# Optimization experiments

Measured on AMD Instinct MI355X. Metric: run time of the kernel, lower is better.

The kernel has to match this reference:

```python
import jax, jax.numpy as jnp
import numpy as np

THRESHOLD = 1.0
DECAY = 0.95
T, B, N_IN = 16, 512, 3072
S1, S2, S3 = 256, 256, 128
E = 8


def _lif_step(v, h):
    # LIF membrane update: decay, integrate, threshold-spike, soft reset.
    v = v * DECAY + h
    spk = (v >= THRESHOLD).astype(v.dtype)
    return spk, v - spk * THRESHOLD


def setup_inputs() -> dict:
    key = jax.random.key(0)
    k_seq, k1, k2, k3 = jax.random.split(key, 4)
    # Binary spike train input (rate-coded), shape (T, B, N_in)
    spike_seq = (jax.random.uniform(k_seq, (T, B, N_IN)) < 0.5).astype(jnp.float32)
    # Expert weights: nn.Linear weight layout is (out, in); init N(0, 0.05)
    W1 = 0.05 * jax.random.normal(k1, (E, S1, N_IN), dtype=jnp.float32)
    W2 = 0.05 * jax.random.normal(k2, (E, S2, S1), dtype=jnp.float32)
    W3 = 0.05 * jax.random.normal(k3, (E, S3, S2), dtype=jnp.float32)
    # Uniform gates 1/num_experts (requires_grad=False buffers in the original)
    g = jnp.full((E,), 1.0 / E, dtype=jnp.float32)
    return {"spike_seq": spike_seq, "W1": W1, "W2": W2, "W3": W3,
            "g1": g, "g2": g, "g3": g}


def reference(spike_seq, W1, W2, W3, g1, g2, g3):
    t, b = spike_seq.shape[0], spike_seq.shape[1]
    x = spike_seq.reshape(t, b, -1)
    e = W1.shape[0]
    dt = x.dtype
    v1 = jnp.zeros((e, b, W1.shape[1]), dt)
    v2 = jnp.zeros((e, b, W2.shape[1]), dt)
    v3 = jnp.zeros((e, b, W3.shape[1]), dt)

    def step(carry, xt):
        v1, v2, v3 = carry
        # stage 1: batched per-expert GEMM + LIF + gated combine
        h1 = jnp.einsum('bi,eoi->ebo', xt, W1)
        spk1, v1 = _lif_step(v1, h1)
        c1 = jnp.einsum('e,ebo->bo', g1, spk1)
        # stage 2
        h2 = jnp.einsum('bi,eoi->ebo', c1, W2)
        spk2, v2 = _lif_step(v2, h2)
        c2 = jnp.einsum('e,ebo->bo', g2, spk2)
        # stage 3
        h3 = jnp.einsum('bi,eoi->ebo', c2, W3)
        spk3, v3 = _lif_step(v3, h3)
        c3 = jnp.einsum('e,ebo->bo', g3, spk3)
        return (v1, v2, v3), (c1, c2, c3)

    _, (s1, s2, s3) = jax.lax.scan(step, (v1, v2, v3), x)
    # time-averaged combined outputs per stage
    return s1.mean(axis=0), s2.mean(axis=0), s3.mean(axis=0)
```

## Files before the change

kernel.cpp:

```cpp
#include <hip/hip_runtime.h>
#include <hip/hip_bf16.h>
#include <cmath>

#define T_STEPS 16
#define BATCH   512
#define N_IN    3072
#define S1      256
#define S2      256
#define S3      128
#define NEXP    8
#define M_ROWS  (T_STEPS * BATCH)
#define MT_ALL  (M_ROWS / 32)

typedef int v4i  __attribute__((ext_vector_type(4)));
typedef int v16i __attribute__((ext_vector_type(16)));
typedef unsigned long long u64;
typedef unsigned int uint32;

__device__ __forceinline__ v4i unpack16_bits(uint32 w16)
{
    v4i d;
    #pragma unroll
    for (int c = 0; c < 4; ++c) {
        uint32 x = (w16 >> (4 * c)) & 0xFu;
        x = x + (x << 7);
        x = x + (x << 14);
        d[c] = (int)(x & 0x01010101u);
    }
    return d;
}

template<int S, int K>
__device__ __forceinline__ void digitize_chunk(
    const float* __restrict__ W, char* __restrict__ Bf, int t)
{
    int lane16 = t & 63;
    int o  = (t >> 6) & (S - 1);
    int kb = t >> ((S == 256) ? 14 : 13);
    int r  = lane16 & 31;
    int qd = lane16 >> 5;
    int e    = r >> 2;
    int limb = r & 3;
    int k0 = kb * 32 + qd * 16;

    const float4* Wp = (const float4*)(W + ((size_t)e * S + o) * K + k0);
    char out[16];
    #pragma unroll
    for (int f4 = 0; f4 < 4; ++f4) {
        float4 w = Wp[f4];
        float ws[4] = {w.x, w.y, w.z, w.w};
        #pragma unroll
        for (int c = 0; c < 4; ++c) {
            long long q = llrint((double)ws[c] * 4294967296.0);
            int d = 0;
            #pragma unroll
            for (int l = 0; l < 4; ++l) {
                int dl = (int)((q + 128) & 255) - 128;
                q = (q - dl) >> 8;
                if (l == limb) d = dl;
            }
            out[f4 * 4 + c] = (char)d;
        }
    }
    *(v4i*)(Bf + (size_t)t * 16) = *(v4i*)out;
}

__global__ __launch_bounds__(256) void prep(
    const float* __restrict__ x,  const float* __restrict__ W1,
    const float* __restrict__ W2, const float* __restrict__ W3,
    u64* __restrict__ bitsT, char* __restrict__ B1f,
    char* __restrict__ B2f,  char* __restrict__ B3f)
{
    const int bid = blockIdx.x;
    const int tid = threadIdx.x;
    if (bid < 98304) {
        int gid = bid * 256 + tid;
        float v = x[gid];
        u64 m = __ballot(v >= 0.5f);
        if ((tid & 63) == 0) {
            int tb = gid / N_IN;
            int k  = gid - tb * N_IN;
            int t  = tb >> 9;
            int b  = tb & 511;
            bitsT[(size_t)(k >> 6) * M_ROWS + (b * 16 + t)] = m;
        }
    } else if (bid < 98304 + 4608) {
        int t    = (bid - 98304) * 256 + tid;
        int l16  = t & 63;
        int tt   = t >> 6;
        int tile = tt % 192;
        int kb   = tt / 192;
        int gr   = tile * 32 + (l16 & 31);
        int qd   = l16 >> 5;
        int limb = gr >> 11;
        int oe   = gr & 2047;
        int o    = oe >> 3;
        int e    = oe & 7;
        int k0   = kb * 32 + qd * 16;
        const float4* Wp = (const float4*)(W1 + ((size_t)e * S1 + o) * N_IN + k0);
        char out[16];
        #pragma unroll
        for (int f4 = 0; f4 < 4; ++f4) {
            float4 w = Wp[f4];
            float ws[4] = {w.x, w.y, w.z, w.w};
            #pragma unroll
            for (int c = 0; c < 4; ++c) {
                long long q = llrint((double)ws[c] * 16777216.0);
                int d0 = (int)((q + 128) & 255) - 128;
                long long q1 = (q - d0) >> 8;
                int d1 = (int)((q1 + 128) & 255) - 128;
                int d2 = (int)((q1 - d1) >> 8);
                int d  = (limb == 0) ? d0 : ((limb == 1) ? d1 : d2);
                out[f4 * 4 + c] = (char)d;
            }
        }
        *(v4i*)(B1f + (size_t)t * 16) = *(v4i*)out;
    } else if (bid < 98304 + 4608 + 512) {
        digitize_chunk<S2, S1>(W2, B2f, (bid - 98304 - 4608) * 256 + tid);
    } else {
        digitize_chunk<S3, S2>(W3, B3f, (bid - 98304 - 4608 - 512) * 256 + tid);
    }
}

__global__ __launch_bounds__(256, 3) void fused_stage1(
    const u64* __restrict__ AT0, const char* __restrict__ Bf,
    const float* __restrict__ g, char* __restrict__ Cf,
    float* __restrict__ Mean)
{
    constexpr int NGR = (N_IN / 32) / 4;
    __shared__ char smem[32768];
    double* hs  = (double*)smem;
    char*  Blds = smem;

    const int tid  = threadIdx.x;
    const int lane = tid & 63;
    const int w    = tid >> 6;
    const int col  = lane & 31;
    const int qd   = lane >> 5;
    const int sh16 = qd * 16;

    const int id    = blockIdx.x;
    const int xcd   = id & 7;
    const int inner = id >> 3;
    const int nblk  = xcd * 8 + (inner >> 5);
    const int mblk  = inner & 31;
    const int m0    = mblk * 256;

    const u64* AT = AT0 + (m0 + w * 64 + col);

    const char* Bsrc = Bf + (size_t)nblk * 1024 + lane * 16;
    char* Bdst0 = Blds + (w * 3) * 1024 + lane * 16;

    v16i acc[2][3];
    #pragma unroll
    for (int mt = 0; mt < 2; ++mt)
        #pragma unroll
        for (int jj = 0; jj < 3; ++jj)
            #pragma unroll
            for (int r = 0; r < 16; ++r) acc[mt][jj][r] = 0;

    u64 areg[2][4];

    auto stageB = [&](int gr, int buf) {
        const char* src = Bsrc + (size_t)(gr * 4 + w) * (192 * 1024);
        char* dst = Bdst0 + buf * 12288;
        #pragma unroll
        for (int jj = 0; jj < 3; ++jj)
            __builtin_amdgcn_global_load_lds(
                (const __attribute__((address_space(1))) uint32*)(src + jj * 65536),
                (__attribute__((address_space(3))) uint32*)(dst + jj * 1024),
                16, 0, 0);
    };
    auto loadA = [&](int gr, int buf) {
        const int kw = gr * 2;
        areg[buf][0] = AT[(size_t)kw * M_ROWS];
        areg[buf][1] = AT[(size_t)kw * M_ROWS + 32];
        areg[buf][2] = AT[(size_t)(kw + 1) * M_ROWS];
        areg[buf][3] = AT[(size_t)(kw + 1) * M_ROWS + 32];
    };

    stageB(0, 0);
    loadA(0, 0);

    auto iter = [&](int gr, int cur, int pf) {
        stageB(gr + 1, pf);
        loadA(gr + 1, pf);
        asm volatile("s_waitcnt vmcnt(7)" ::: "memory");
        __builtin_amdgcn_sched_barrier(0);
        __builtin_amdgcn_s_barrier();
        const char* bb = Blds + cur * 12288 + lane * 16;
        __builtin_amdgcn_s_setprio(1);
        #pragma unroll
        for (int kbl = 0; kbl < 4; ++kbl) {
            v4i Bfr[3];
            #pragma unroll
            for (int jj = 0; jj < 3; ++jj)
                Bfr[jj] = *(const v4i*)(bb + (kbl * 3 + jj) * 1024);
            const int kwl = kbl >> 1;
            v4i af[2];
            #pragma unroll
            for (int mt = 0; mt < 2; ++mt) {
                u64 a = areg[cur][kwl * 2 + mt];
                uint32 dw = (kbl & 1) ? (uint32)(a >> 32) : (uint32)a;
                af[mt] = unpack16_bits(dw >> sh16);
            }
            #pragma unroll
            for (int mt = 0; mt < 2; ++mt)
                #pragma unroll
                for (int jj = 0; jj < 3; ++jj)
                    acc[mt][jj] = __builtin_amdgcn_mfma_i32_32x32x32_i8(
                        af[mt], Bfr[jj], acc[mt][jj], 0, 0, 0);
        }
        __builtin_amdgcn_s_setprio(0);
        __builtin_amdgcn_s_barrier();
    };

    for (int gp = 0; gp < NGR; gp += 2) {
        iter(gp + 0, 0, 1);
        iter(gp + 1, 1, 0);
    }

    const double sc = 1.0 / 16777216.0;
    auto write_hs = [&](int wl) {
        #pragma unroll
        for (int mt = 0; mt < 2; ++mt)
            #pragma unroll
            for (int reg = 0; reg < 16; ++reg) {
                int r  = wl * 64 + mt * 32 + (reg & 3) + 8 * (reg >> 2) + 4 * qd;
                int lo = acc[mt][0][reg] + (acc[mt][1][reg] << 8);
                double d = ((double)lo + 65536.0 * (double)acc[mt][2][reg]) * sc;
                hs[r * 32 + col] = d;
            }
    };
    const int b_loc = tid >> 5;
    const int oe    = tid & 31;
    const int o_loc = oe >> 3;
    const int e     = tid & 7;
    const float ge  = g[e];
    const int og    = nblk * 4 + o_loc;
    const int kb_a   = og >> 5;
    const int qd_a   = (og >> 4) & 1;
    const int byte_a = og & 15;

    auto lif_pass = [&](int pass) {
        const int bg = mblk * 16 + pass * 8 + b_loc;
        double v = 0.0;
        float gacc = 0.0f;
        #pragma unroll
        for (int t = 0; t < T_STEPS; ++t) {
            double h  = hs[(b_loc * 16 + t) * 32 + oe];
            double vv = v * 0.95 + h;
            int spk = (vv >= 1.0) ? 1 : 0;
            v = vv - (double)spk;
            float gs = ge * (float)spk;
            gs += __shfl_xor(gs, 1);
            gs += __shfl_xor(gs, 2);
            gs += __shfl_xor(gs, 4);
            gacc += gs;
            int cnt = spk;
            cnt += __shfl_xor(cnt, 1);
            cnt += __shfl_xor(cnt, 2);
            cnt += __shfl_xor(cnt, 4);
            if (e == 0) {
                int mp = bg * 16 + t;
                int lane_a = (mp & 31) + 32 * qd_a;
                Cf[(((size_t)kb_a * MT_ALL + (mp >> 5)) * 64 + lane_a) * 16 + byte_a]
                    = (char)cnt;
            }
        }
        if (e == 0) Mean[(size_t)bg * S1 + og] = gacc * 0.0625f;
    };

    __syncthreads();
    if (w < 2) write_hs(w);
    __syncthreads();
    lif_pass(0);
    __syncthreads();
    if (w >= 2) write_hs(w - 2);
    __syncthreads();
    lif_pass(1);
}

template<int K, int S, int SHIFT, bool WRITEC, int NBLK, int MINW>
__global__ __launch_bounds__(256, MINW) void fused_stage(
    const char* __restrict__ Ap, const char* __restrict__ Bf,
    const float* __restrict__ g, char* __restrict__ Cf,
    float* __restrict__ Mean)
{
    constexpr int KI = K / 64;
    static_assert(KI % 2 == 0, "frag path wants even KI");
    constexpr int NT = S;
    constexpr int NS = NBLK / 8;
    __shared__ double hs[256][16];

    const int tid  = threadIdx.x;
    const int lane = tid & 63;
    const int w    = tid >> 6;
    const int col  = lane & 31;
    const int qd   = lane >> 5;
    const int wm   = w * 64;

    const int id    = blockIdx.x;
    const int xcd   = id & 7;
    const int inner = id >> 3;
    const int nblk  = xcd * NS + (inner >> 5);
    const int mblk  = inner & 31;
    const int m0    = mblk * 256;

    const int nt0 = nblk * 2;
    const char* Bbase = Bf + ((size_t)nt0 * 64 + lane) * 16;

    v16i acc[2][2];
    #pragma unroll
    for (int i = 0; i < 2; ++i)
        #pragma unroll
        for (int j = 0; j < 2; ++j)
            #pragma unroll
            for (int r = 0; r < 16; ++r) acc[i][j][r] = 0;

    auto loadB = [&](int kb, int jj) -> v4i {
        return *(const v4i*)(Bbase + (size_t)kb * (NT * 1024) + jj * 1024);
    };
    const int mt0 = (m0 + wm) >> 5;
    const char* Abase = Ap + ((size_t)mt0 * 64 + lane) * 16;
    auto loadA = [&](int kb, int ii) -> v4i {
        return *(const v4i*)(Abase + (size_t)kb * (MT_ALL * 1024) + ii * 1024);
    };

    v4i Ab[2][4];
    v4i Bb[2][4];

    #pragma unroll
    for (int ks = 0; ks < 2; ++ks) {
        Ab[0][ks * 2 + 0] = loadA(ks, 0);
        Ab[0][ks * 2 + 1] = loadA(ks, 1);
        #pragma unroll
        for (int jj = 0; jj < 2; ++jj)
            Bb[0][ks * 2 + jj] = loadB(ks, jj);
    }

    auto body = [&](int it, int cur, int pf) {
        const int itp = it + 1;
        #pragma unroll
        for (int ks = 0; ks < 2; ++ks) {
            Ab[pf][ks * 2 + 0] = loadA(itp * 2 + ks, 0);
            Ab[pf][ks * 2 + 1] = loadA(itp * 2 + ks, 1);
            #pragma unroll
            for (int jj = 0; jj < 2; ++jj)
                Bb[pf][ks * 2 + jj] = loadB(itp * 2 + ks, jj);
        }
        #pragma unroll
        for (int ks = 0; ks < 2; ++ks)
            #pragma unroll
            for (int jj = 0; jj < 2; ++jj) {
                acc[0][jj] = __builtin_amdgcn_mfma_i32_32x32x32_i8(Ab[cur][ks*2+0], Bb[cur][ks*2+jj], acc[0][jj], 0,0,0);
                acc[1][jj] = __builtin_amdgcn_mfma_i32_32x32x32_i8(Ab[cur][ks*2+1], Bb[cur][ks*2+jj], acc[1][jj], 0,0,0);
            }
    };
    for (int it = 0; it < KI; it += 2) {
        body(it + 0, 0, 1);
        body(it + 1, 1, 0);
    }

    const double sbase = 1.0 / (double)(1ll << SHIFT);
    #pragma unroll
    for (int j = 0; j < 2; ++j) {
        const int oe = j * 8 + (col >> 2);
        #pragma unroll
        for (int i = 0; i < 2; ++i) {
            #pragma unroll
            for (int reg = 0; reg < 16; ++reg) {
                int a = acc[i][j][reg];
                int s01 = a + (__shfl_xor(a, 1) << 8);
                int s23 = __shfl_xor(s01, 2);
                double d = ((double)s01 + 65536.0 * (double)s23) * sbase;
                if ((col & 3) == 0) {
                    int m = wm + i * 32 + (reg & 3) + 8 * (reg >> 2) + 4 * qd;
                    hs[m][oe] = d;
                }
            }
        }
    }
    __syncthreads();

    const int b_loc  = tid >> 4;
    const int o_loc  = (tid >> 3) & 1;
    const int e      = tid & 7;
    const int oe     = o_loc * 8 + e;
    const float ge   = g[e];
    const int bg = mblk * 16 + b_loc;
    const int og = nblk * 2 + o_loc;

    const int kb_a   = og >> 5;
    const int qd_a   = (og >> 4) & 1;
    const int byte_a = og & 15;

    double v = 0.0;
    float gacc = 0.0f;
    #pragma unroll
    for (int t = 0; t < T_STEPS; ++t) {
        double h  = hs[b_loc * 16 + t][oe];
        double vv = v * 0.95 + h;
        int spk = (vv >= 1.0) ? 1 : 0;
        v = vv - (double)spk;
        float gs = ge * (float)spk;
        gs += __shfl_xor(gs, 1);
        gs += __shfl_xor(gs, 2);
        gs += __shfl_xor(gs, 4);
        gacc += gs;
        if (WRITEC) {
            int cnt = spk;
            cnt += __shfl_xor(cnt, 1);
            cnt += __shfl_xor(cnt, 2);
            cnt += __shfl_xor(cnt, 4);
            if (e == 0) {
                int mp = bg * 16 + t;
                int lane_a = (mp & 31) + 32 * qd_a;
                Cf[(((size_t)kb_a * MT_ALL + (mp >> 5)) * 64 + lane_a) * 16 + byte_a]
                    = (char)cnt;
            }
        }
    }
    if (e == 0) Mean[(size_t)bg * S + og] = gacc * 0.0625f;
}

extern "C" void kernel_launch(void* const* d_in, const int* in_sizes, int n_in,
                              void* d_out, int out_size, void* d_ws, size_t ws_size,
                              hipStream_t stream) {
    const float* x  = (const float*)d_in[0];
    const float* W1 = (const float*)d_in[1];
    const float* W2 = (const float*)d_in[2];
    const float* W3 = (const float*)d_in[3];
    const float* g1 = (const float*)d_in[4];
    const float* g2 = (const float*)d_in[5];
    const float* g3 = (const float*)d_in[6];
    float* out = (float*)d_out;

    char* ws = (char*)d_ws;
    u64*  AbitsT = (u64*)ws;
    char* B1f    = ws + 4194304ull;
    char* B2f    = ws + 25165824ull;
    char* B3f    = ws + 28311552ull;
    char* c1f    = ws + 30408704ull;
    char* c2f    = ws + 34603008ull;

    dim3 blk(256);

    prep<<<98304 + 4608 + 512 + 256, blk, 0, stream>>>(
        x, W1, W2, W3, AbitsT, B1f, B2f, B3f);

    fused_stage1<<<32 * 64, blk, 0, stream>>>(AbitsT, B1f, g1, c1f, out);

    fused_stage<S1, S2, 35, true,  128, 3><<<32 * 128, blk, 0, stream>>>(
        c1f, B2f, g2, c2f, out + BATCH * S1);
    fused_stage<S2, S3, 35, false, 64, 3><<<32 * 64, blk, 0, stream>>>(
        c2f, B3f, g3, nullptr, out + BATCH * (S1 + S2));
}
```

Baseline: 449.8 us.

## Halve stage-1 M tile to 128 rows, double grid, raise occupancy to 4

Stage-1 now has each block cover 128 rows instead of 256, with each wave computing one 32-row M tile instead of two. The grid doubles to 4096 blocks and the launch bound rises from 3 to 4 blocks per CU, with fewer accumulator registers per wave. The two-pass LIF epilogue collapses into a single pass. This trades B-operand reuse (each B tile is now loaded by twice as many blocks) for more parallelism and occupancy to hide latency.

```diff
diff --git a/kernel.cpp b/kernel.cpp
--- a/kernel.cpp
+++ b/kernel.cpp
@@ -122,7 +122,7 @@
     }
 }
 
-__global__ __launch_bounds__(256, 3) void fused_stage1(
+__global__ __launch_bounds__(256, 4) void fused_stage1(
     const u64* __restrict__ AT0, const char* __restrict__ Bf,
     const float* __restrict__ g, char* __restrict__ Cf,
     float* __restrict__ Mean)
@@ -142,24 +142,22 @@
     const int id    = blockIdx.x;
     const int xcd   = id & 7;
     const int inner = id >> 3;
-    const int nblk  = xcd * 8 + (inner >> 5);
-    const int mblk  = inner & 31;
-    const int m0    = mblk * 256;
-
-    const u64* AT = AT0 + (m0 + w * 64 + col);
+    const int nblk  = xcd * 8 + (inner >> 6);
+    const int mblk  = inner & 63;
+    const int m0    = mblk * 128;
+
+    const u64* AT = AT0 + (m0 + w * 32 + col);
 
     const char* Bsrc = Bf + (size_t)nblk * 1024 + lane * 16;
     char* Bdst0 = Blds + (w * 3) * 1024 + lane * 16;
 
-    v16i acc[2][3];
-    #pragma unroll
-    for (int mt = 0; mt < 2; ++mt)
-        #pragma unroll
-        for (int jj = 0; jj < 3; ++jj)
-            #pragma unroll
-            for (int r = 0; r < 16; ++r) acc[mt][jj][r] = 0;
-
-    u64 areg[2][4];
+    v16i acc[3];
+    #pragma unroll
+    for (int jj = 0; jj < 3; ++jj)
+        #pragma unroll
+        for (int r = 0; r < 16; ++r) acc[jj][r] = 0;
+
+    u64 a0[2], a1[2];
 
     auto stageB = [&](int gr, int buf) {
         const char* src = Bsrc + (size_t)(gr * 4 + w) * (192 * 1024);
@@ -172,11 +170,8 @@
                 16, 0, 0);
     };
     auto loadA = [&](int gr, int buf) {
-        const int kw = gr * 2;
-        areg[buf][0] = AT[(size_t)kw * M_ROWS];
-        areg[buf][1] = AT[(size_t)kw * M_ROWS + 32];
-        areg[buf][2] = AT[(size_t)(kw + 1) * M_ROWS];
-        areg[buf][3] = AT[(size_t)(kw + 1) * M_ROWS + 32];
+        a0[buf] = AT[(size_t)(gr * 2 + 0) * M_ROWS];
+        a1[buf] = AT[(size_t)(gr * 2 + 1) * M_ROWS];
     };
 
     stageB(0, 0);
@@ -185,7 +180,7 @@
     auto iter = [&](int gr, int cur, int pf) {
         stageB(gr + 1, pf);
         loadA(gr + 1, pf);
-        asm volatile("s_waitcnt vmcnt(7)" ::: "memory");
+        asm volatile("s_waitcnt vmcnt(5)" ::: "memory");
         __builtin_amdgcn_sched_barrier(0);
         __builtin_amdgcn_s_barrier();
         const char* bb = Blds + cur * 12288 + lane * 16;
@@ -196,20 +191,13 @@
             #pragma unroll
             for (int jj = 0; jj < 3; ++jj)
                 Bfr[jj] = *(const v4i*)(bb + (kbl * 3 + jj) * 1024);
-            const int kwl = kbl >> 1;
-            v4i af[2];
-            #pragma unroll
-            for (int mt = 0; mt < 2; ++mt) {
-                u64 a = areg[cur][kwl * 2 + mt];
-                uint32 dw = (kbl & 1) ? (uint32)(a >> 32) : (uint32)a;
-                af[mt] = unpack16_bits(dw >> sh16);
-            }
-            #pragma unroll
-            for (int mt = 0; mt < 2; ++mt)
-                #pragma unroll
-                for (int jj = 0; jj < 3; ++jj)
-                    acc[mt][jj] = __builtin_amdgcn_mfma_i32_32x32x32_i8(
-                        af[mt], Bfr[jj], acc[mt][jj], 0, 0, 0);
+            u64 a = (kbl >> 1) ? a1[cur] : a0[cur];
+            uint32 dw = (kbl & 1) ? (uint32)(a >> 32) : (uint32)a;
+            v4i af = unpack16_bits(dw >> sh16);
+            #pragma unroll
+            for (int jj = 0; jj < 3; ++jj)
+                acc[jj] = __builtin_amdgcn_mfma_i32_32x32x32_i8(
+                    af, Bfr[jj], acc[jj], 0, 0, 0);
         }
         __builtin_amdgcn_s_setprio(0);
         __builtin_amdgcn_s_barrier();
@@ -221,64 +209,52 @@
     }
 
     const double sc = 1.0 / 16777216.0;
-    auto write_hs = [&](int wl) {
-        #pragma unroll
-        for (int mt = 0; mt < 2; ++mt)
-            #pragma unroll
-            for (int reg = 0; reg < 16; ++reg) {
-                int r  = wl * 64 + mt * 32 + (reg & 3) + 8 * (reg >> 2) + 4 * qd;
-                int lo = acc[mt][0][reg] + (acc[mt][1][reg] << 8);
-                double d = ((double)lo + 65536.0 * (double)acc[mt][2][reg]) * sc;
-                hs[r * 32 + col] = d;
-            }
-    };
+    __syncthreads();
+    #pragma unroll
+    for (int reg = 0; reg < 16; ++reg) {
+        int r  = w * 32 + (reg & 3) + 8 * (reg >> 2) + 4 * qd;
+        int lo = acc[0][reg] + (acc[1][reg] << 8);
+        double d = ((double)lo + 65536.0 * (double)acc[2][reg]) * sc;
+        hs[r * 32 + col] = d;
+    }
+    __syncthreads();
+
     const int b_loc = tid >> 5;
     const int oe    = tid & 31;
     const int o_loc = oe >> 3;
     const int e     = tid & 7;
     const float ge  = g[e];
+    const int bg    = mblk * 8 + b_loc;
     const int og    = nblk * 4 + o_loc;
     const int kb_a   = og >> 5;
     const int qd_a   = (og >> 4) & 1;
     const int byte_a = og & 15;
 
-    auto lif_pass = [&](int pass) {
-        const int bg = mblk * 16 + pass * 8 + b_loc;
-        double v = 0.0;
-        float gacc = 0.0f;
-        #pragma unroll
-        for (int t = 0; t < T_STEPS; ++t) {
-            double h  = hs[(b_loc * 16 + t) * 32 + oe];
-            double vv = v * 0.95 + h;
-            int spk = (vv >= 1.0) ? 1 : 0;
-            v = vv - (double)spk;
-            float gs = ge * (float)spk;
-            gs += __shfl_xor(gs, 1);
-            gs += __shfl_xor(gs, 2);
-            gs += __shfl_xor(gs, 4);
-            gacc += gs;
-            int cnt = spk;
-            cnt += __shfl_xor(cnt, 1);
-            cnt += __shfl_xor(cnt, 2);
-            cnt += __shfl_xor(cnt, 4);
-            if (e == 0) {
-                int mp = bg * 16 + t;
-                int lane_a = (mp & 31) + 32 * qd_a;
-                Cf[(((size_t)kb_a * MT_ALL + (mp >> 5)) * 64 + lane_a) * 16 + byte_a]
-                    = (char)cnt;
-            }
-        }
-        if (e == 0) Mean[(size_t)bg * S1 + og] = gacc * 0.0625f;
-    };
-
-    __syncthreads();
-    if (w < 2) write_hs(w);
-    __syncthreads();
-    lif_pass(0);
-    __syncthreads();
-    if (w >= 2) write_hs(w - 2);
-    __syncthreads();
-    lif_pass(1);
+    double v = 0.0;
+    float gacc = 0.0f;
+    #pragma unroll
+    for (int t = 0; t < T_STEPS; ++t) {
+        double h  = hs[(b_loc * 16 + t) * 32 + oe];
+        double vv = v * 0.95 + h;
+        int spk = (vv >= 1.0) ? 1 : 0;
+        v = vv - (double)spk;
+        float gs = ge * (float)spk;
+        gs += __shfl_xor(gs, 1);
+        gs += __shfl_xor(gs, 2);
+        gs += __shfl_xor(gs, 4);
+        gacc += gs;
+        int cnt = spk;
+        cnt += __shfl_xor(cnt, 1);
+        cnt += __shfl_xor(cnt, 2);
+        cnt += __shfl_xor(cnt, 4);
+        if (e == 0) {
+            int mp = bg * 16 + t;
+            int lane_a = (mp & 31) + 32 * qd_a;
+            Cf[(((size_t)kb_a * MT_ALL + (mp >> 5)) * 64 + lane_a) * 16 + byte_a]
+                = (char)cnt;
+        }
+    }
+    if (e == 0) Mean[(size_t)bg * S1 + og] = gacc * 0.0625f;
 }
 
 template<int K, int S, int SHIFT, bool WRITEC, int NBLK, int MINW>
@@ -449,7 +425,7 @@
     prep<<<98304 + 4608 + 512 + 256, blk, 0, stream>>>(
         x, W1, W2, W3, AbitsT, B1f, B2f, B3f);
 
-    fused_stage1<<<32 * 64, blk, 0, stream>>>(AbitsT, B1f, g1, c1f, out);
+    fused_stage1<<<64 * 64, blk, 0, stream>>>(AbitsT, B1f, g1, c1f, out);
 
     fused_stage<S1, S2, 35, true,  128, 3><<<32 * 128, blk, 0, stream>>>(
         c1f, B2f, g2, c2f, out + BATCH * S1);
```

Result: slower. 459.6 us (+2.2%).
